# Optimization experiments

Hardware: AMD Instinct MI355X
Metric: run time of the kernel (lower is better)

The kernel has to match this reference:

```python
import jax, jax.numpy as jnp
import numpy as np

USER_NUM = 100000
ITEM_NUM = 50000
N = USER_NUM + ITEM_NUM
EMB = 64
NNZ = 1000000
COEF_A, COEF_B, COEF_C = 0.1, 0.1, 0.0


def setup_inputs() -> dict:
    key = jax.random.key(0)
    ks = jax.random.split(key, 11)
    return {
        "user_emb": jax.random.normal(ks[0], (USER_NUM, EMB), jnp.float32) * 0.1,
        "item_emb": jax.random.normal(ks[1], (ITEM_NUM, EMB), jnp.float32) * 0.1,
        "adj_rows": jax.random.randint(ks[2], (NNZ,), 0, N, jnp.int32),
        "adj_cols": jax.random.randint(ks[3], (NNZ,), 0, N, jnp.int32),
        "adj_vals": jax.random.uniform(ks[4], (NNZ,), jnp.float32),
        "aj_rows": jax.random.randint(ks[5], (NNZ,), 0, N, jnp.int32),
        "aj_cols": jax.random.randint(ks[6], (NNZ,), 0, N, jnp.int32),
        "aj_vals": jax.random.uniform(ks[7], (NNZ,), jnp.float32),
        "ai_rows": jax.random.randint(ks[8], (NNZ,), 0, N, jnp.int32),
        "ai_cols": jax.random.randint(ks[9], (NNZ,), 0, N, jnp.int32),
        "ai_vals": jax.random.uniform(ks[10], (NNZ,), jnp.float32),
    }


def _spmm(rows, cols, vals, x):
    # COO sparse (N x N) @ dense (N x d) -> (N x d)
    gathered = vals[:, None] * x[cols]  # [nnz, d]
    return jax.ops.segment_sum(gathered, rows, num_segments=N)


def reference(user_emb, item_emb, adj_rows, adj_cols, adj_vals,
              aj_rows, aj_cols, aj_vals, ai_rows, ai_cols, ai_vals):
    ego = jnp.concatenate([user_emb, item_emb], axis=0)  # [N, d]

    def hop(x, coef):
        e = _spmm(adj_rows, adj_cols, adj_vals, x)
        m = _spmm(aj_rows, aj_cols, aj_vals, e)
        m = _spmm(ai_rows, ai_cols, ai_vals, m)
        return (1.0 + coef) * e - coef * m

    e1 = hop(ego, COEF_A)
    e2 = hop(e1, COEF_B)
    e3 = hop(e2, COEF_C)
    all_emb = (ego + e1 + e2 + e3) / 4.0  # mean over stacked layer dim
    return all_emb[:USER_NUM], all_emb[USER_NUM:]
```

## Files before the change

### kernel.cpp

```cpp
#include <hip/hip_runtime.h>
#include <hip/hip_fp16.h>

#define USER_NUM 100000
#define ITEM_NUM 50000
#define NROWS    150000
#define EMB      64
#define ELEMS    (NROWS * EMB)
#define BROWS    1024
#define NBM      147
#define NBT      (3 * NBM)
#define RPSTRIDE (NROWS + 1)
#define P1_CHUNK 4096
#define LENB     64


__device__ __forceinline__ uint2 ldnt_u2(const void* p) {
    unsigned long long v = __builtin_nontemporal_load((const unsigned long long*)p);
    uint2 r; r.x = (unsigned)v; r.y = (unsigned)(v >> 32); return r;
}
__device__ __forceinline__ void stnt_u64(void* p, unsigned long long v) {
    __builtin_nontemporal_store(v, (unsigned long long*)p);
}


__global__ void bucket_hist(const int* __restrict__ r0, const int* __restrict__ r1,
                            const int* __restrict__ r2, int n0, int n1, int n2,
                            int* __restrict__ bcnt) {
    const int m = blockIdx.y;
    const int* rows = (m == 0) ? r0 : (m == 1) ? r1 : r2;
    const int  nnz  = (m == 0) ? n0 : (m == 1) ? n1 : n2;
    __shared__ int cnt[NBM];
    for (int i = threadIdx.x; i < NBM; i += blockDim.x) cnt[i] = 0;
    __syncthreads();
    for (int i = blockIdx.x * blockDim.x + threadIdx.x; i < nnz; i += gridDim.x * blockDim.x)
        atomicAdd(&cnt[rows[i] >> 10], 1);
    __syncthreads();
    int* g = bcnt + m * NBM;
    for (int i = threadIdx.x; i < NBM; i += blockDim.x) {
        int c = cnt[i];
        if (c) atomicAdd(&g[i], c);
    }
}

__global__ void bucket_scan(const int* __restrict__ bcnt, int* __restrict__ bbase,
                            int* __restrict__ bfill) {
    __shared__ int sh[512];
    int t = threadIdx.x;
    sh[t] = (t < NBT) ? bcnt[t] : 0;
    __syncthreads();
    for (int o = 1; o < 512; o <<= 1) {
        int v = (t >= o) ? sh[t - o] : 0;
        __syncthreads();
        sh[t] += v;
        __syncthreads();
    }
    int ex = t ? sh[t - 1] : 0;
    if (t <= NBT) bbase[t] = ex;
    if (t < NBT)  bfill[t] = ex;
}

__global__ void bucket_bin(const int* __restrict__ r0, const int* __restrict__ c0, const float* __restrict__ v0,
                           const int* __restrict__ r1, const int* __restrict__ c1, const float* __restrict__ v1,
                           const int* __restrict__ r2, const int* __restrict__ c2, const float* __restrict__ v2,
                           int n0, int n1, int n2,
                           int* __restrict__ bfill, int2* __restrict__ tmp) {
    const int m = blockIdx.y;
    const int*   rows = (m == 0) ? r0 : (m == 1) ? r1 : r2;
    const int*   cols = (m == 0) ? c0 : (m == 1) ? c1 : c2;
    const float* vals = (m == 0) ? v0 : (m == 1) ? v1 : v2;
    const int    nnz  = (m == 0) ? n0 : (m == 1) ? n1 : n2;

    int start = blockIdx.x * P1_CHUNK;
    if (start >= nnz) return;
    int end = start + P1_CHUNK;
    if (end > nnz) end = nnz;

    __shared__ int lcnt[NBM];
    __shared__ int lbase[NBM];
    for (int i = threadIdx.x; i < NBM; i += blockDim.x) lcnt[i] = 0;
    __syncthreads();
    for (int i = start + threadIdx.x; i < end; i += blockDim.x)
        atomicAdd(&lcnt[rows[i] >> 10], 1);
    __syncthreads();
    int* gf = bfill + m * NBM;
    for (int i = threadIdx.x; i < NBM; i += blockDim.x) {
        int c = lcnt[i];
        lbase[i] = c ? atomicAdd(&gf[i], c) : 0;
    }
    __syncthreads();
    for (int i = threadIdx.x; i < NBM; i += blockDim.x) lcnt[i] = 0;
    __syncthreads();
    for (int i = start + threadIdx.x; i < end; i += blockDim.x) {
        int r = rows[i];
        int b = r >> 10;
        int pos = lbase[b] + atomicAdd(&lcnt[b], 1);
        tmp[pos] = make_int2(((r & 1023) << 18) | cols[i], __float_as_int(vals[i]));
    }
}

__global__ void bucket_sort(const int2* __restrict__ tmp, const int* __restrict__ bbase,
                            int2* __restrict__ pk, int* __restrict__ rpg) {
    int gb = blockIdx.x;
    int m  = gb / NBM;
    int lb = gb - m * NBM;
    int base = bbase[gb];
    int next = bbase[gb + 1];
    int r0 = lb << 10;
    int cover = NROWS - r0; if (cover > BROWS) cover = BROWS;

    __shared__ int cnt[BROWS];
    __shared__ int tsum[256];
    int t = threadIdx.x;
    for (int i = t; i < BROWS; i += 256) cnt[i] = 0;
    __syncthreads();
    for (int i = base + t; i < next; i += 256) atomicAdd(&cnt[tmp[i].x >> 18], 1);
    __syncthreads();
    int c0 = cnt[4*t], c1 = cnt[4*t+1], c2 = cnt[4*t+2], c3 = cnt[4*t+3];
    int s = c0 + c1 + c2 + c3;
    tsum[t] = s;
    __syncthreads();
    for (int o = 1; o < 256; o <<= 1) {
        int v = (t >= o) ? tsum[t - o] : 0;
        __syncthreads();
        tsum[t] += v;
        __syncthreads();
    }
    int ex = t ? tsum[t - 1] : 0;
    cnt[4*t] = ex; cnt[4*t+1] = ex + c0; cnt[4*t+2] = ex + c0 + c1; cnt[4*t+3] = ex + c0 + c1 + c2;
    __syncthreads();
    int* rp = rpg + m * RPSTRIDE;
    for (int k = t; k < cover; k += 256) rp[r0 + k] = base + cnt[k];
    if (t == 0) rp[r0 + cover] = next;
    __syncthreads();
    for (int i = base + t; i < next; i += 256) {
        int2 e2 = tmp[i];
        int r = e2.x >> 18;
        int pos = base + atomicAdd(&cnt[r], 1);
        pk[pos] = make_int2(e2.x & 0x3FFFF, e2.y);
    }
}


__global__ void len_hist(const int* __restrict__ rpg, int* __restrict__ lhist) {
    int m = blockIdx.y;
    const int* rp = rpg + m * RPSTRIDE;
    __shared__ int sh[LENB];
    int t = threadIdx.x;
    if (t < LENB) sh[t] = 0;
    __syncthreads();
    int r = blockIdx.x * blockDim.x + t;
    if (r < NROWS) {
        int len = rp[r + 1] - rp[r]; if (len > LENB - 1) len = LENB - 1;
        atomicAdd(&sh[len], 1);
    }
    __syncthreads();
    if (t < LENB) {
        int c = sh[t];
        if (c) atomicAdd(&lhist[m * LENB + t], c);
    }
}

__global__ void len_scan(const int* __restrict__ lhist, int* __restrict__ lfill) {
    __shared__ int sh[3 * LENB];
    int t = threadIdx.x;
    if (t < 3 * LENB) sh[t] = lhist[t];
    __syncthreads();
    if (t < 3) {
        int run = 0;
        for (int b = 0; b < LENB; ++b) { int v = sh[t * LENB + b]; sh[t * LENB + b] = run; run += v; }
    }
    __syncthreads();
    if (t < 3 * LENB) lfill[t] = sh[t];
}

__global__ void len_scatter(const int* __restrict__ rpg, int* __restrict__ lfill,
                            int* __restrict__ perm) {
    int m = blockIdx.y;
    const int* rp = rpg + m * RPSTRIDE;
    __shared__ int lcnt[LENB];
    __shared__ int lbase[LENB];
    int t = threadIdx.x;
    if (t < LENB) lcnt[t] = 0;
    __syncthreads();
    int r = blockIdx.x * blockDim.x + t;
    int len = -1;
    if (r < NROWS) {
        len = rp[r + 1] - rp[r]; if (len > LENB - 1) len = LENB - 1;
        atomicAdd(&lcnt[len], 1);
    }
    __syncthreads();
    if (t < LENB) {
        int c = lcnt[t];
        lbase[t] = c ? atomicAdd(&lfill[m * LENB + t], c) : 0;
        lcnt[t] = 0;
    }
    __syncthreads();
    if (r < NROWS) {
        int pos = lbase[len] + atomicAdd(&lcnt[len], 1);
        perm[m * NROWS + pos] = r;
    }
}


__global__ void lgcn_init4(const float* __restrict__ ue,
                           const float* __restrict__ ie,
                           __half* __restrict__ x0) {
    int i4 = blockIdx.x * blockDim.x + threadIdx.x;
    int base = i4 << 2;
    int row = base >> 6;
    float4 v = (row < USER_NUM)
        ? ((const float4*)ue)[i4]
        : ((const float4*)ie)[i4 - (USER_NUM * EMB >> 2)];
    __half2 h01 = __floats2half2_rn(v.x, v.y);
    __half2 h23 = __floats2half2_rn(v.z, v.w);
    uint2 packed;
    packed.x = *(const unsigned int*)&h01;
    packed.y = *(const unsigned int*)&h23;
    ((uint2*)x0)[i4] = packed;
}


__device__ __forceinline__ void fma_h4(float4& A, float v, const __half* xp) {
    uint2 u = *(const uint2*)xp;
    float2 f0 = __half22float2(*(__half2*)&u.x);
    float2 f1 = __half22float2(*(__half2*)&u.y);
    A.x = fmaf(v, f0.x, A.x); A.y = fmaf(v, f0.y, A.y);
    A.z = fmaf(v, f1.x, A.z); A.w = fmaf(v, f1.y, A.w);
}

__device__ __forceinline__ float4 row_dot_g(const int* __restrict__ rp,
                                            const int2* __restrict__ pk,
                                            const __half* __restrict__ x,
                                            int row, int k4) {
    int s = rp[row], e = rp[row + 1];
    float4 A = make_float4(0.f, 0.f, 0.f, 0.f);
    float4 B = make_float4(0.f, 0.f, 0.f, 0.f);
    float4 Cc = make_float4(0.f, 0.f, 0.f, 0.f);
    float4 D = make_float4(0.f, 0.f, 0.f, 0.f);
    int i = s;
    for (; i + 3 < e; i += 4) {
        int2 p0 = pk[i], p1 = pk[i + 1], p2 = pk[i + 2], p3 = pk[i + 3];
        const __half* a0 = x + (p0.x << 6) + k4;
        const __half* a1 = x + (p1.x << 6) + k4;
        const __half* a2 = x + (p2.x << 6) + k4;
        const __half* a3 = x + (p3.x << 6) + k4;
        fma_h4(A, __int_as_float(p0.y), a0);
        fma_h4(B, __int_as_float(p1.y), a1);
        fma_h4(Cc, __int_as_float(p2.y), a2);
        fma_h4(D, __int_as_float(p3.y), a3);
    }
    for (; i < e; ++i) {
        int2 p = pk[i];
        fma_h4(A, __int_as_float(p.y), x + (p.x << 6) + k4);
    }
    A.x += B.x + Cc.x + D.x;
    A.y += B.y + Cc.y + D.y;
    A.z += B.z + Cc.z + D.z;
    A.w += B.w + Cc.w + D.w;
    return A;
}

__device__ __forceinline__ unsigned long long pack_h4(float a, float b, float c, float d) {
    __half2 h0 = __floats2half2_rn(a, b);
    __half2 h1 = __floats2half2_rn(c, d);
    return ((unsigned long long)(*(unsigned*)&h1) << 32) | *(unsigned*)&h0;
}

__global__ void spmm_plain(const int* __restrict__ rp, const int2* __restrict__ pk,
                           const int* __restrict__ perm,
                           const __half* __restrict__ x, __half* __restrict__ out) {
    int lane = threadIdx.x & 63;
    int W = (blockIdx.x << 2) + (threadIdx.x >> 6);
    int g = lane >> 4, k4 = (lane & 15) << 2;
    int row = perm[(W << 2) + g];
    float4 a = row_dot_g(rp, pk, x, row, k4);
    stnt_u64(out + (row << 6) + k4, pack_h4(a.x, a.y, a.z, a.w));
}

__global__ void spmm_combine(const int* __restrict__ rp, const int2* __restrict__ pk,
                             const int* __restrict__ perm,
                             const __half* __restrict__ tx, const __half* __restrict__ ex,
                             __half* __restrict__ xout, float coef) {
    int lane = threadIdx.x & 63;
    int W = (blockIdx.x << 2) + (threadIdx.x >> 6);
    int g = lane >> 4, k4 = (lane & 15) << 2;
    int row = perm[(W << 2) + g];
    float4 mm = row_dot_g(rp, pk, tx, row, k4);
    int off = (row << 6) + k4;
    uint2 u = ldnt_u2(ex + off);
    float2 e0 = __half22float2(*(__half2*)&u.x);
    float2 e1 = __half22float2(*(__half2*)&u.y);
    float cp = 1.0f + coef;
    stnt_u64(xout + off, pack_h4(cp * e0.x - coef * mm.x, cp * e0.y - coef * mm.y,
                                 cp * e1.x - coef * mm.z, cp * e1.y - coef * mm.w));
}

__global__ void spmm_final(const int* __restrict__ rp, const int2* __restrict__ pk,
                           const int* __restrict__ perm,
                           const __half* __restrict__ x2, const __half* __restrict__ x0,
                           const __half* __restrict__ x1, float* __restrict__ acc) {
    int lane = threadIdx.x & 63;
    int W = (blockIdx.x << 2) + (threadIdx.x >> 6);
    int g = lane >> 4, k4 = (lane & 15) << 2;
    int row = perm[(W << 2) + g];
    float4 e3 = row_dot_g(rp, pk, x2, row, k4);
    int off = (row << 6) + k4;
    uint2 u0 = ldnt_u2(x0 + off);
    uint2 u1 = ldnt_u2(x1 + off);
    uint2 u2 = ldnt_u2(x2 + off);
    float2 a0 = __half22float2(*(__half2*)&u0.x), b0 = __half22float2(*(__half2*)&u0.y);
    float2 a1 = __half22float2(*(__half2*)&u1.x), b1 = __half22float2(*(__half2*)&u1.y);
    float2 a2 = __half22float2(*(__half2*)&u2.x), b2 = __half22float2(*(__half2*)&u2.y);
    float sx = 0.25f * (a0.x + a1.x + a2.x + e3.x);
    float sy = 0.25f * (a0.y + a1.y + a2.y + e3.y);
    float sz = 0.25f * (b0.x + b1.x + b2.x + e3.z);
    float sw = 0.25f * (b0.y + b1.y + b2.y + e3.w);
    unsigned long long lo, hi;
    float2 p0 = make_float2(sx, sy), p1 = make_float2(sz, sw);
    __builtin_memcpy(&lo, &p0, 8);
    __builtin_memcpy(&hi, &p1, 8);
    stnt_u64(acc + off, lo);
    stnt_u64(acc + off + 2, hi);
}


extern "C" void kernel_launch(void* const* d_in, const int* in_sizes, int n_in,
                              void* d_out, int out_size, void* d_ws, size_t ws_size,
                              hipStream_t stream) {
    const float* ue = (const float*)d_in[0];
    const float* ie = (const float*)d_in[1];
    const int*   R[3] = { (const int*)d_in[2], (const int*)d_in[5], (const int*)d_in[8] };
    const int*   C[3] = { (const int*)d_in[3], (const int*)d_in[6], (const int*)d_in[9] };
    const float* V[3] = { (const float*)d_in[4], (const float*)d_in[7], (const float*)d_in[10] };
    const int    NZ[3] = { in_sizes[2], in_sizes[5], in_sizes[8] };
    const int    NZT = NZ[0] + NZ[1] + NZ[2];

    float* acc = (float*)d_out;

    char* cur = (char*)d_ws;
    int2* pk    = (int2*)cur;  cur += (size_t)NZT * sizeof(int2);
    int*  rpg   = (int*)cur;   cur += (((size_t)3 * RPSTRIDE * 4 + 7) & ~7ull);
    int*  perm  = (int*)cur;   cur += (size_t)3 * NROWS * sizeof(int);
    int*  bcnt  = (int*)cur;   cur += ((NBT * 4 + 7) & ~7ull);
    int*  bbase = (int*)cur;   cur += (((NBT + 1) * 4 + 7) & ~7ull);
    int*  bfill = (int*)cur;   cur += ((NBT * 4 + 7) & ~7ull);
    int*  lhist = (int*)cur;   cur += 3 * LENB * sizeof(int);
    int*  lfill = (int*)cur;   cur += 3 * LENB * sizeof(int);
    __half* x0 = (__half*)cur; cur += (size_t)ELEMS * sizeof(__half);
    __half* x1 = (__half*)cur; cur += (size_t)ELEMS * sizeof(__half);
    __half* x2 = (__half*)cur; cur += (size_t)ELEMS * sizeof(__half);
    __half* tE = (__half*)cur; cur += (size_t)ELEMS * sizeof(__half);
    __half* tT = (__half*)cur; cur += (size_t)ELEMS * sizeof(__half);
    int2* tmp  = (int2*)tE;
    (void)ws_size;

    const int* rpAdj = rpg;
    const int* rpAj  = rpg + RPSTRIDE;
    const int* rpAi  = rpg + 2 * RPSTRIDE;
    const int* pAdj = perm;
    const int* pAj  = perm + NROWS;
    const int* pAi  = perm + 2 * NROWS;

    int maxNZ = NZ[0]; if (NZ[1] > maxNZ) maxNZ = NZ[1]; if (NZ[2] > maxNZ) maxNZ = NZ[2];

    hipMemsetAsync(bcnt, 0, NBT * sizeof(int), stream);
    hipMemsetAsync(lhist, 0, 3 * LENB * sizeof(int), stream);
    dim3 gH(256, 3);
    bucket_hist<<<gH, 256, 0, stream>>>(R[0], R[1], R[2], NZ[0], NZ[1], NZ[2], bcnt);
    bucket_scan<<<1, 512, 0, stream>>>(bcnt, bbase, bfill);
    dim3 gB((maxNZ + P1_CHUNK - 1) / P1_CHUNK, 3);
    bucket_bin<<<gB, 256, 0, stream>>>(R[0], C[0], V[0], R[1], C[1], V[1], R[2], C[2], V[2],
                                       NZ[0], NZ[1], NZ[2], bfill, tmp);
    bucket_sort<<<NBT, 256, 0, stream>>>(tmp, bbase, pk, rpg);

    dim3 gL((NROWS + 255) / 256, 3);
    len_hist   <<<gL, 256, 0, stream>>>(rpg, lhist);
    len_scan   <<<1, 256, 0, stream>>>(lhist, lfill);
    len_scatter<<<gL, 256, 0, stream>>>(rpg, lfill, perm);

    const int BLK = 256;
    const int gridI = (ELEMS / 4) / BLK;
    const int gridS = NROWS / 16;

    lgcn_init4<<<gridI, BLK, 0, stream>>>(ue, ie, x0);

    spmm_plain  <<<gridS, BLK, 0, stream>>>(rpAdj, pk, pAdj, x0, tE);
    spmm_plain  <<<gridS, BLK, 0, stream>>>(rpAj,  pk, pAj,  tE, tT);
    spmm_combine<<<gridS, BLK, 0, stream>>>(rpAi,  pk, pAi,  tT, tE, x1, 0.1f);

    spmm_plain  <<<gridS, BLK, 0, stream>>>(rpAdj, pk, pAdj, x1, tE);
    spmm_plain  <<<gridS, BLK, 0, stream>>>(rpAj,  pk, pAj,  tE, tT);
    spmm_combine<<<gridS, BLK, 0, stream>>>(rpAi,  pk, pAi,  tT, tE, x2, 0.1f);

    spmm_final  <<<gridS, BLK, 0, stream>>>(rpAdj, pk, pAdj, x2, x0, x1, acc);
}
```

Baseline: 443.0 us.

## Pack CSR column and value into 32-bit words, unroll gather by eight

Each CSR entry is compressed from an 8-byte int2 holding column and fp32 value into one 32-bit word: an 18-bit column plus a 14-bit truncated half-precision value, decoded in the SpMM inner loop. This halves index/value traffic and workspace footprint for all nine SpMM passes. The inner loop is also unrolled to eight gathers to raise memory-level parallelism, and the row permutation order is reversed so longest rows are scheduled first. The value encoding drops two mantissa bits beyond fp16, which adds approximation error in the weights.

```diff
diff --git a/kernel.cpp b/kernel.cpp
--- a/kernel.cpp
+++ b/kernel.cpp
@@ -99,7 +99,7 @@
 }
 
 __global__ void bucket_sort(const int2* __restrict__ tmp, const int* __restrict__ bbase,
-                            int2* __restrict__ pk, int* __restrict__ rpg) {
+                            unsigned* __restrict__ pk, int* __restrict__ rpg) {
     int gb = blockIdx.x;
     int m  = gb / NBM;
     int lb = gb - m * NBM;
@@ -136,7 +136,11 @@
         int2 e2 = tmp[i];
         int r = e2.x >> 18;
         int pos = base + atomicAdd(&cnt[r], 1);
-        pk[pos] = make_int2(e2.x & 0x3FFFF, e2.y);
+        float f = __int_as_float(e2.y);
+        __half h = __float2half_rn(f);
+        unsigned short hb = *(unsigned short*)&h;
+        unsigned enc = ((unsigned)(e2.x & 0x3FFFF) << 14) | ((unsigned)(hb + 2u) >> 2);
+        pk[pos] = enc;
     }
 }
 
@@ -167,7 +171,7 @@
     __syncthreads();
     if (t < 3) {
         int run = 0;
-        for (int b = 0; b < LENB; ++b) { int v = sh[t * LENB + b]; sh[t * LENB + b] = run; run += v; }
+        for (int b = LENB - 1; b >= 0; --b) { int v = sh[t * LENB + b]; sh[t * LENB + b] = run; run += v; }
     }
     __syncthreads();
     if (t < 3 * LENB) lfill[t] = sh[t];
@@ -220,8 +224,13 @@
 }
 
 
-__device__ __forceinline__ void fma_h4(float4& A, float v, const __half* xp) {
-    uint2 u = *(const uint2*)xp;
+__device__ __forceinline__ float dec_val(unsigned u) {
+    unsigned short hb = (unsigned short)((u & 0x3FFFu) << 2);
+    __half h = *(__half*)&hb;
+    return __half2float(h);
+}
+
+__device__ __forceinline__ void fma_h4u(float4& A, float v, uint2 u) {
     float2 f0 = __half22float2(*(__half2*)&u.x);
     float2 f1 = __half22float2(*(__half2*)&u.y);
     A.x = fmaf(v, f0.x, A.x); A.y = fmaf(v, f0.y, A.y);
@@ -229,7 +238,7 @@
 }
 
 __device__ __forceinline__ float4 row_dot_g(const int* __restrict__ rp,
-                                            const int2* __restrict__ pk,
+                                            const unsigned* __restrict__ pk,
                                             const __half* __restrict__ x,
                                             int row, int k4) {
     int s = rp[row], e = rp[row + 1];
@@ -238,20 +247,41 @@
     float4 Cc = make_float4(0.f, 0.f, 0.f, 0.f);
     float4 D = make_float4(0.f, 0.f, 0.f, 0.f);
     int i = s;
+    for (; i + 7 < e; i += 8) {
+        unsigned u0 = pk[i+0], u1 = pk[i+1], u2 = pk[i+2], u3 = pk[i+3];
+        unsigned u4 = pk[i+4], u5 = pk[i+5], u6 = pk[i+6], u7 = pk[i+7];
+        uint2 g0 = *(const uint2*)(x + ((u0 >> 14) << 6) + k4);
+        uint2 g1 = *(const uint2*)(x + ((u1 >> 14) << 6) + k4);
+        uint2 g2 = *(const uint2*)(x + ((u2 >> 14) << 6) + k4);
+        uint2 g3 = *(const uint2*)(x + ((u3 >> 14) << 6) + k4);
+        uint2 g4 = *(const uint2*)(x + ((u4 >> 14) << 6) + k4);
+        uint2 g5 = *(const uint2*)(x + ((u5 >> 14) << 6) + k4);
+        uint2 g6 = *(const uint2*)(x + ((u6 >> 14) << 6) + k4);
+        uint2 g7 = *(const uint2*)(x + ((u7 >> 14) << 6) + k4);
+        fma_h4u(A, dec_val(u0), g0);
+        fma_h4u(B, dec_val(u1), g1);
+        fma_h4u(Cc, dec_val(u2), g2);
+        fma_h4u(D, dec_val(u3), g3);
+        fma_h4u(A, dec_val(u4), g4);
+        fma_h4u(B, dec_val(u5), g5);
+        fma_h4u(Cc, dec_val(u6), g6);
+        fma_h4u(D, dec_val(u7), g7);
+    }
     for (; i + 3 < e; i += 4) {
-        int2 p0 = pk[i], p1 = pk[i + 1], p2 = pk[i + 2], p3 = pk[i + 3];
-        const __half* a0 = x + (p0.x << 6) + k4;
-        const __half* a1 = x + (p1.x << 6) + k4;
-        const __half* a2 = x + (p2.x << 6) + k4;
-        const __half* a3 = x + (p3.x << 6) + k4;
-        fma_h4(A, __int_as_float(p0.y), a0);
-        fma_h4(B, __int_as_float(p1.y), a1);
-        fma_h4(Cc, __int_as_float(p2.y), a2);
-        fma_h4(D, __int_as_float(p3.y), a3);
+        unsigned u0 = pk[i+0], u1 = pk[i+1], u2 = pk[i+2], u3 = pk[i+3];
+        uint2 g0 = *(const uint2*)(x + ((u0 >> 14) << 6) + k4);
+        uint2 g1 = *(const uint2*)(x + ((u1 >> 14) << 6) + k4);
+        uint2 g2 = *(const uint2*)(x + ((u2 >> 14) << 6) + k4);
+        uint2 g3 = *(const uint2*)(x + ((u3 >> 14) << 6) + k4);
+        fma_h4u(A, dec_val(u0), g0);
+        fma_h4u(B, dec_val(u1), g1);
+        fma_h4u(Cc, dec_val(u2), g2);
+        fma_h4u(D, dec_val(u3), g3);
     }
     for (; i < e; ++i) {
-        int2 p = pk[i];
-        fma_h4(A, __int_as_float(p.y), x + (p.x << 6) + k4);
+        unsigned u0 = pk[i];
+        uint2 g0 = *(const uint2*)(x + ((u0 >> 14) << 6) + k4);
+        fma_h4u(A, dec_val(u0), g0);
     }
     A.x += B.x + Cc.x + D.x;
     A.y += B.y + Cc.y + D.y;
@@ -266,7 +296,7 @@
     return ((unsigned long long)(*(unsigned*)&h1) << 32) | *(unsigned*)&h0;
 }
 
-__global__ void spmm_plain(const int* __restrict__ rp, const int2* __restrict__ pk,
+__global__ void spmm_plain(const int* __restrict__ rp, const unsigned* __restrict__ pk,
                            const int* __restrict__ perm,
                            const __half* __restrict__ x, __half* __restrict__ out) {
     int lane = threadIdx.x & 63;
@@ -277,7 +307,7 @@
     stnt_u64(out + (row << 6) + k4, pack_h4(a.x, a.y, a.z, a.w));
 }
 
-__global__ void spmm_combine(const int* __restrict__ rp, const int2* __restrict__ pk,
+__global__ void spmm_combine(const int* __restrict__ rp, const unsigned* __restrict__ pk,
                              const int* __restrict__ perm,
                              const __half* __restrict__ tx, const __half* __restrict__ ex,
                              __half* __restrict__ xout, float coef) {
@@ -295,7 +325,7 @@
                                  cp * e1.x - coef * mm.z, cp * e1.y - coef * mm.w));
 }
 
-__global__ void spmm_final(const int* __restrict__ rp, const int2* __restrict__ pk,
+__global__ void spmm_final(const int* __restrict__ rp, const unsigned* __restrict__ pk,
                            const int* __restrict__ perm,
                            const __half* __restrict__ x2, const __half* __restrict__ x0,
                            const __half* __restrict__ x1, float* __restrict__ acc) {
@@ -338,7 +368,7 @@
     float* acc = (float*)d_out;
 
     char* cur = (char*)d_ws;
-    int2* pk    = (int2*)cur;  cur += (size_t)NZT * sizeof(int2);
+    unsigned* pk = (unsigned*)cur;  cur += (((size_t)NZT * 4 + 7) & ~7ull);
     int*  rpg   = (int*)cur;   cur += (((size_t)3 * RPSTRIDE * 4 + 7) & ~7ull);
     int*  perm  = (int*)cur;   cur += (size_t)3 * NROWS * sizeof(int);
     int*  bcnt  = (int*)cur;   cur += ((NBT * 4 + 7) & ~7ull);
```

Result: faster. 419.9 us (-5.2%).
